# Kernel optimization log

Hardware: AMD Instinct MI355X
Metric: run time of the kernel (lower is better)

## Reference

```python
import jax, jax.numpy as jnp
import numpy as np

N = 512            # n_inputs (even)
L = N              # n_layers = n_inputs
PE = N // 2        # couplers per even column
PO = N // 2 - 1    # couplers per odd column
TWO_PI = 6.283185307179586


def _ste_clamp(theta):
    # clamp_ste: clamp value to [0, 2*pi], straight-through gradient
    c = jnp.clip(theta, 0.0, TWO_PI)
    return theta + jax.lax.stop_gradient(c - theta)


def _phase(theta):
    return jax.lax.complex(jnp.cos(theta), jnp.sin(theta))


def _pc_even(M, theta):
    # phase shifter on upper arm of each even pair: rows 0,2,4,...
    return M.at[0::2].multiply(_phase(theta)[:, None])


def _pc_odd(M, theta):
    # phase shifter on upper arm of each odd pair: rows 1,3,...,N-3
    return M.at[1:N - 1:2].multiply(_phase(theta)[:, None])


def _mmi_coeffs(loss, imb):
    # lossy, imbalanced 2x2 MMI: a*[[t, i r],[i r, t]]
    a = jnp.sqrt(1.0 - loss)
    t = a * jnp.sqrt(0.5 + imb)
    r = a * jnp.sqrt(0.5 - imb)
    ir = jax.lax.complex(jnp.zeros_like(r), r)
    return t, ir


def _mmi_even(M, loss, imb):
    t, ir = _mmi_coeffs(loss, imb)
    Mp = M.reshape(PE, 2, N)                       # pairs (0,1),(2,3),...
    top, bot = Mp[:, 0], Mp[:, 1]
    nt = t[:, None] * top + ir[:, None] * bot
    nb = ir[:, None] * top + t[:, None] * bot
    return jnp.stack([nt, nb], axis=1).reshape(N, N)


def _mmi_odd(M, loss, imb):
    t, ir = _mmi_coeffs(loss, imb)
    Mi = M[1:N - 1].reshape(PO, 2, N)              # pairs (1,2),(3,4),...
    top, bot = Mi[:, 0], Mi[:, 1]
    nt = t[:, None] * top + ir[:, None] * bot
    nb = ir[:, None] * top + t[:, None] * bot
    mid = jnp.stack([nt, nb], axis=1).reshape(N - 2, N)
    return jnp.concatenate([M[:1], mid, M[N - 1:]], axis=0)


def _forward(pc_even_phases, pc_odd_phases, pc_out_phases,
             mmi_loss_even, mmi_imb_even, mmi_loss_odd, mmi_imb_odd):
    pe = _ste_clamp(pc_even_phases).reshape(L // 2, 2, PE)
    po = _ste_clamp(pc_odd_phases).reshape(L // 2, 2, PO)
    le = mmi_loss_even.reshape(L // 2, 2, PE)
    ie = mmi_imb_even.reshape(L // 2, 2, PE)
    lo = mmi_loss_odd.reshape(L // 2, 2, PO)
    io = mmi_imb_odd.reshape(L // 2, 2, PO)

    def step(M, p):
        pe_, le_, ie_, po_, lo_, io_ = p
        for j in range(2):  # two even PC+MMI columns
            M = _pc_even(M, pe_[j])
            M = _mmi_even(M, le_[j], ie_[j])
        for j in range(2):  # two odd PC+MMI columns
            M = _pc_odd(M, po_[j])
            M = _mmi_odd(M, lo_[j], io_[j])
        return M, None

    M0 = jnp.eye(N, dtype=jnp.complex64)
    M, _ = jax.lax.scan(jax.checkpoint(step), M0, (pe, le, ie, po, lo, io))
    # output phase column on every wire
    return M * _phase(_ste_clamp(pc_out_phases))[:, None]


def setup_inputs() -> dict:
    key = jax.random.key(0)
    ks = jax.random.split(key, 7)
    return {
        "pc_even_phases": jax.random.uniform(ks[0], (L, PE), jnp.float32, 0.0, TWO_PI),
        "pc_odd_phases": jax.random.uniform(ks[1], (L, PO), jnp.float32, 0.0, TWO_PI),
        "pc_out_phases": jax.random.uniform(ks[2], (N,), jnp.float32, 0.0, TWO_PI),
        "mmi_loss_even": jax.random.uniform(ks[3], (L, PE), jnp.float32, 0.0, 0.05),
        "mmi_imb_even": jax.random.uniform(ks[4], (L, PE), jnp.float32, -0.05, 0.05),
        "mmi_loss_odd": jax.random.uniform(ks[5], (L, PO), jnp.float32, 0.0, 0.05),
        "mmi_imb_odd": jax.random.uniform(ks[6], (L, PO), jnp.float32, -0.05, 0.05),
    }


def reference(pc_even_phases, pc_odd_phases, pc_out_phases,
              mmi_loss_even, mmi_imb_even, mmi_loss_odd, mmi_imb_odd):
    return _forward(pc_even_phases, pc_odd_phases, pc_out_phases,
                    mmi_loss_even, mmi_imb_even, mmi_loss_odd, mmi_imb_odd)
```

## Files before the change

kernel.cpp:

```cpp
#include <hip/hip_runtime.h>
#include <hip/hip_fp16.h>

#define TWO_PI_F 6.283185307179586f

__device__ __forceinline__ float clamp02pi(float x) {
    return fminf(fmaxf(x, 0.0f), TWO_PI_F);
}

__device__ __forceinline__ float2 cmul(const float2 a, const float2 b) {
    return make_float2(a.x * b.x - a.y * b.y, a.x * b.y + a.y * b.x);
}
__device__ __forceinline__ float2 cadd(const float2 a, const float2 b) {
    return make_float2(a.x + b.x, a.y + b.y);
}
__device__ __forceinline__ float2 cscale(const float s, const float2 a) {
    return make_float2(s * a.x, s * a.y);
}
__device__ __forceinline__ float2 imul(const float r, const float2 e) {
    return make_float2(-r * e.y, r * e.x);
}
__device__ __forceinline__ float2 cfma(const float2 acc, const float2 a, const float2 b) {
    return make_float2(acc.x + a.x * b.x - a.y * b.y,
                       acc.y + a.x * b.y + a.y * b.x);
}

__device__ __forceinline__ float2 h2f(const unsigned u) {
    return __half22float2(__builtin_bit_cast(__half2, u));
}
__device__ __forceinline__ unsigned f2h(const float2 f) {
    return __builtin_bit_cast(unsigned, __float22half2_rn(f));
}

__device__ __forceinline__ void compose_row_w(
    const float4 (*sE)[72], const float4 (*sO)[72], const int r, const int P0,
    float4& h0, float4& h1)
{
    float2 f0, f1, f2, f3;
    if (r == 0) {
        const float4 q1 = sE[1][0], q0 = sE[0][0];
        const float2 e1 = make_float2(q1.x, q1.y);
        const float2 e0 = make_float2(q0.x, q0.y);
        const float2 v2 = cscale(q1.z, e1);
        const float2 v3 = make_float2(0.0f, q1.w);
        f2 = cadd(cmul(v2, cscale(q0.z, e0)), cmul(v3, imul(q0.w, e0)));
        f3 = cadd(cmul(v2, make_float2(0.0f, q0.w)), cscale(q0.z, v3));
        f0 = make_float2(0.0f, 0.0f);
        f1 = make_float2(0.0f, 0.0f);
    } else {
        const int pidx = ((r - 1) >> 1) - P0;
        const int qidx = min(((r - 1) >> 1) + 1, 255) - P0;
        const float4 qO1 = sO[1][pidx], qO0 = sO[0][pidx];
        const float2 eO1 = make_float2(qO1.x, qO1.y);
        const float2 eO0 = make_float2(qO0.x, qO0.y);
        float2 w1, w2;
        if (r & 1) { w1 = cscale(qO1.z, eO1); w2 = make_float2(0.0f, qO1.w); }
        else       { w1 = imul(qO1.w, eO1);   w2 = make_float2(qO1.z, 0.0f); }
        const float2 u1 = cadd(cmul(w1, cscale(qO0.z, eO0)),
                               cmul(w2, imul(qO0.w, eO0)));
        const float2 u2 = cadd(cmul(w1, make_float2(0.0f, qO0.w)),
                               cscale(qO0.z, w2));
        const float4 qE1p = sE[1][pidx], qE1q = sE[1][qidx];
        const float4 qE0p = sE[0][pidx], qE0q = sE[0][qidx];
        const float2 eE1p = make_float2(qE1p.x, qE1p.y);
        const float2 eE1q = make_float2(qE1q.x, qE1q.y);
        const float2 eE0p = make_float2(qE0p.x, qE0p.y);
        const float2 eE0q = make_float2(qE0q.x, qE0q.y);
        const float2 v0 = cmul(u1, imul(qE1p.w, eE1p));
        const float2 v1 = cscale(qE1p.z, u1);
        const float2 v2 = cmul(u2, cscale(qE1q.z, eE1q));
        const float2 v3 = cmul(u2, make_float2(0.0f, qE1q.w));
        f0 = cadd(cmul(v0, cscale(qE0p.z, eE0p)), cmul(v1, imul(qE0p.w, eE0p)));
        f1 = cadd(cmul(v0, make_float2(0.0f, qE0p.w)), cscale(qE0p.z, v1));
        f2 = cadd(cmul(v2, cscale(qE0q.z, eE0q)), cmul(v3, imul(qE0q.w, eE0q)));
        f3 = cadd(cmul(v2, make_float2(0.0f, qE0q.w)), cscale(qE0q.z, v3));
    }
    h0 = make_float4(f0.x, f0.y, f1.x, f1.y);
    h1 = make_float4(f2.x, f2.y, f3.x, f3.y);
}

__global__ __launch_bounds__(256) void compose8q_kernel(
    const float* __restrict__ pe, const float* __restrict__ po,
    const float* __restrict__ le, const float* __restrict__ ie,
    const float* __restrict__ lo, const float* __restrict__ io,
    uint4* __restrict__ Mch8)
{
    const int q = blockIdx.x;
    const int j = q >> 2;
    const int quarter = q & 3;
    const int R0 = 128 * quarter;
    const int P0 = (quarter == 0) ? 0 : ((R0 - 3) >> 1);
    const int t = threadIdx.x;

    __shared__ float4 sE[4][72];
    __shared__ float4 sO[4][72];
    __shared__ float4 B4[2][134][2];

    for (int it = t; it < 576; it += 256) {
        const int half = it / 288;
        const int rem  = it % 288;
        const int sub  = rem / 72;
        const int w    = rem % 72;
        const int p    = P0 + w;
        if (p > 255) continue;
        if (half == 0) {
            const int idx = (4 * j + sub) * 256 + p;
            float s, c;
            __sincosf(clamp02pi(pe[idx]), &s, &c);
            const float a = sqrtf(1.0f - le[idx]);
            sE[sub][w] = make_float4(c, s, a * sqrtf(0.5f + ie[idx]),
                                           a * sqrtf(0.5f - ie[idx]));
        } else {
            float4 qv = make_float4(1.0f, 0.0f, 1.0f, 0.0f);
            if (p < 255) {
                const int odx = (4 * j + sub) * 255 + p;
                float s, c;
                __sincosf(clamp02pi(po[odx]), &s, &c);
                const float a = sqrtf(1.0f - lo[odx]);
                qv = make_float4(c, s, a * sqrtf(0.5f + io[odx]),
                                       a * sqrtf(0.5f - io[odx]));
            }
            sO[sub][w] = qv;
        }
    }
    __syncthreads();

    for (int it = t; it < 268; it += 256) {
        const int s = it / 134, slot = it % 134;
        const int row = R0 - 2 + slot;
        if (row >= 0 && row <= 511) {
            float4 h0, h1;
            compose_row_w(&sE[2 * s], &sO[2 * s], row, P0, h0, h1);
            B4[s][slot][0] = h0;
            B4[s][slot][1] = h1;
        }
    }
    __syncthreads();

    if (t < 128) {
        const int r = R0 + t;
        const int base = (r & 1) ? (r - 1) : (r - 2);
        const int sr = t + 2;
        const float4 wv0 = B4[1][sr][0], wv1 = B4[1][sr][1];
        const float2 w0 = make_float2(wv0.x, wv0.y), w1 = make_float2(wv0.z, wv0.w);
        const float2 w2 = make_float2(wv1.x, wv1.y), w3 = make_float2(wv1.z, wv1.w);
        float2 p0 = make_float2(0.f,0.f), p1 = p0, p2 = p0, p3 = p0,
               p4 = p0, p5 = p0, p6 = p0, p7 = p0;
        {   const int k = min(max(base, 0), 511) - (R0 - 2);
            const float4 a = B4[0][k][0], b = B4[0][k][1];
            p0 = cfma(p0, w0, make_float2(a.x, a.y));
            p1 = cfma(p1, w0, make_float2(a.z, a.w));
            p2 = cfma(p2, w0, make_float2(b.x, b.y));
            p3 = cfma(p3, w0, make_float2(b.z, b.w)); }
        {   const int k = min(max(base + 1, 0), 511) - (R0 - 2);
            const float4 a = B4[0][k][0], b = B4[0][k][1];
            p2 = cfma(p2, w1, make_float2(a.x, a.y));
            p3 = cfma(p3, w1, make_float2(a.z, a.w));
            p4 = cfma(p4, w1, make_float2(b.x, b.y));
            p5 = cfma(p5, w1, make_float2(b.z, b.w)); }
        {   const int k = min(max(base + 2, 0), 511) - (R0 - 2);
            const float4 a = B4[0][k][0], b = B4[0][k][1];
            p2 = cfma(p2, w2, make_float2(a.x, a.y));
            p3 = cfma(p3, w2, make_float2(a.z, a.w));
            p4 = cfma(p4, w2, make_float2(b.x, b.y));
            p5 = cfma(p5, w2, make_float2(b.z, b.w)); }
        {   const int k = min(max(base + 3, 0), 511) - (R0 - 2);
            const float4 a = B4[0][k][0], b = B4[0][k][1];
            p4 = cfma(p4, w3, make_float2(a.x, a.y));
            p5 = cfma(p5, w3, make_float2(a.z, a.w));
            p6 = cfma(p6, w3, make_float2(b.x, b.y));
            p7 = cfma(p7, w3, make_float2(b.z, b.w)); }
        uint4* dst = Mch8 + (size_t)j * 1024 + (r & 1) * 512 + (r >> 1);
        dst[0]   = make_uint4(f2h(p0), f2h(p1), f2h(p2), f2h(p3));
        dst[256] = make_uint4(f2h(p4), f2h(p5), f2h(p6), f2h(p7));
    }
}

__device__ __forceinline__ float2 hrow4(const uint4 q, const float2 a,
                                        const float2 b, const float2 d,
                                        const float2 e, float2 acc)
{
    acc = cfma(acc, h2f(q.x), a);
    acc = cfma(acc, h2f(q.y), b);
    acc = cfma(acc, h2f(q.z), d);
    acc = cfma(acc, h2f(q.w), e);
    return acc;
}

__global__ __launch_bounds__(256) void mesh8h_kernel(
    const uint4* __restrict__ Mch,
    const float* __restrict__ pout,
    float* __restrict__ out, const int out_size)
{
    const int t   = threadIdx.x;
    const int col = blockIdx.x;

    __shared__ float4 S[2][260];

    float2 T = make_float2((2 * t     == col) ? 1.0f : 0.0f, 0.0f);
    float2 B = make_float2((2 * t + 1 == col) ? 1.0f : 0.0f, 0.0f);
    S[0][t + 2] = make_float4(T.x, T.y, B.x, B.y);
    if (t < 2) {
        const float4 z = make_float4(0.f, 0.f, 0.f, 0.f);
        S[0][t] = z; S[1][t] = z;
        S[0][258 + t] = z; S[1][258 + t] = z;
    }

    uint4 c0 = Mch[t],       c1 = Mch[256 + t],
          c2 = Mch[512 + t], c3 = Mch[768 + t];
    __syncthreads();

#pragma unroll 1
    for (int i = 0; i < 128; ++i) {
        const int nb = ((i + 1) & 127) * 1024 + t;
        const uint4 n0 = Mch[nb],       n1 = Mch[nb + 256],
                    n2 = Mch[nb + 512], n3 = Mch[nb + 768];

        const float4* SS = S[i & 1];
        const float4 s0 = SS[t], s1 = SS[t + 1], s3 = SS[t + 3], s4 = SS[t + 4];

        float2 YT = hrow4(c0, make_float2(s0.x, s0.y), make_float2(s0.z, s0.w),
                              make_float2(s1.x, s1.y), make_float2(s1.z, s1.w),
                          make_float2(0.f, 0.f));
        YT = hrow4(c1, T, B,
                       make_float2(s3.x, s3.y), make_float2(s3.z, s3.w), YT);
        float2 YB = hrow4(c2, make_float2(s1.x, s1.y), make_float2(s1.z, s1.w),
                              T, B, make_float2(0.f, 0.f));
        YB = hrow4(c3, make_float2(s3.x, s3.y), make_float2(s3.z, s3.w),
                       make_float2(s4.x, s4.y), make_float2(s4.z, s4.w), YB);
        T = YT; B = YB;
        S[(i + 1) & 1][t + 2] = make_float4(T.x, T.y, B.x, B.y);
        __syncthreads();

        c0 = n0; c1 = n1; c2 = n2; c3 = n3;
    }

    float s0p, c0p, s1p, c1p;
    __sincosf(clamp02pi(pout[2 * t]),     &s0p, &c0p);
    __sincosf(clamp02pi(pout[2 * t + 1]), &s1p, &c1p);
    const int i0 = (2 * t) * 512 + col;
    const int i1 = i0 + 512;
    if (i0 < out_size) out[i0] = c0p * T.x - s0p * T.y;
    if (i1 < out_size) out[i1] = c1p * B.x - s1p * B.y;
}

__global__ __launch_bounds__(256) void mesh_kernel(
    const float* __restrict__ pe, const float* __restrict__ po,
    const float* __restrict__ pout,
    const float* __restrict__ le, const float* __restrict__ ie,
    const float* __restrict__ lo, const float* __restrict__ io,
    float* __restrict__ out, const int out_size)
{
    const int p = threadIdx.x;
    const int b = blockIdx.x;

    __shared__ float4 P[2][256];

    P[0][p] = (p == b) ? make_float4(1.0f, 0.0f, 0.0f, 0.0f)
                       : make_float4(0.0f, 0.0f, 0.0f, 0.0f);
    P[1][p] = (p == b) ? make_float4(0.0f, 0.0f, 1.0f, 0.0f)
                       : make_float4(0.0f, 0.0f, 0.0f, 0.0f);

#pragma unroll 1
    for (int i = 0; i < 256; ++i) {
        const int e0 = (2 * i) * 256 + p, e1 = e0 + 256;
        const float pe0 = pe[e0], le0 = le[e0], ie0 = ie[e0];
        const float pe1 = pe[e1], le1 = le[e1], ie1 = ie[e1];
        float po0 = 0.0f, lo0 = 0.0f, io0 = 0.0f;
        float po1 = 0.0f, lo1 = 0.0f, io1 = 0.0f;
        if (p < 255) {
            const int o0 = (2 * i) * 255 + p, o1 = o0 + 255;
            po0 = po[o0]; lo0 = lo[o0]; io0 = io[o0];
            po1 = po[o1]; lo1 = lo[o1]; io1 = io[o1];
        }

        float4 v0 = P[0][p];
        float4 v1 = P[1][p];
#pragma unroll
        for (int j = 0; j < 2; ++j) {
            float s, c;
            __sincosf(clamp02pi(j ? pe1 : pe0), &s, &c);
            const float a  = sqrtf(1.0f - (j ? le1 : le0));
            const float tt = a * sqrtf(0.5f + (j ? ie1 : ie0));
            const float rr = a * sqrtf(0.5f - (j ? ie1 : ie0));
            {
                const float ptr_ = c * v0.x - s * v0.y;
                const float pti_ = c * v0.y + s * v0.x;
                v0 = make_float4(tt * ptr_ - rr * v0.w, tt * pti_ + rr * v0.z,
                                 tt * v0.z - rr * pti_, tt * v0.w + rr * ptr_);
            }
            {
                const float ptr_ = c * v1.x - s * v1.y;
                const float pti_ = c * v1.y + s * v1.x;
                v1 = make_float4(tt * ptr_ - rr * v1.w, tt * pti_ + rr * v1.z,
                                 tt * v1.z - rr * pti_, tt * v1.w + rr * ptr_);
            }
        }
        P[0][p] = v0;
        P[1][p] = v1;
        __syncthreads();

        if (p < 255) {
            float2 top0 = make_float2(P[0][p].z, P[0][p].w);
            float2 bot0 = make_float2(P[0][p + 1].x, P[0][p + 1].y);
            float2 top1 = make_float2(P[1][p].z, P[1][p].w);
            float2 bot1 = make_float2(P[1][p + 1].x, P[1][p + 1].y);
#pragma unroll
            for (int j = 0; j < 2; ++j) {
                float s, c;
                __sincosf(clamp02pi(j ? po1 : po0), &s, &c);
                const float a  = sqrtf(1.0f - (j ? lo1 : lo0));
                const float tt = a * sqrtf(0.5f + (j ? io1 : io0));
                const float rr = a * sqrtf(0.5f - (j ? io1 : io0));
                {
                    const float ptr_ = c * top0.x - s * top0.y;
                    const float pti_ = c * top0.y + s * top0.x;
                    const float nbx = tt * bot0.x - rr * pti_;
                    const float nby = tt * bot0.y + rr * ptr_;
                    top0 = make_float2(tt * ptr_ - rr * bot0.y, tt * pti_ + rr * bot0.x);
                    bot0 = make_float2(nbx, nby);
                }
                {
                    const float ptr_ = c * top1.x - s * top1.y;
                    const float pti_ = c * top1.y + s * top1.x;
                    const float nbx = tt * bot1.x - rr * pti_;
                    const float nby = tt * bot1.y + rr * ptr_;
                    top1 = make_float2(tt * ptr_ - rr * bot1.y, tt * pti_ + rr * bot1.x);
                    bot1 = make_float2(nbx, nby);
                }
            }
            P[0][p].z = top0.x; P[0][p].w = top0.y;
            P[0][p + 1].x = bot0.x; P[0][p + 1].y = bot0.y;
            P[1][p].z = top1.x; P[1][p].w = top1.y;
            P[1][p + 1].x = bot1.x; P[1][p + 1].y = bot1.y;
        }
        __syncthreads();
    }

    const float4 v0 = P[0][p];
    const float4 v1 = P[1][p];
    float s0, c0, s1, c1;
    __sincosf(clamp02pi(pout[2 * p]),     &s0, &c0);
    __sincosf(clamp02pi(pout[2 * p + 1]), &s1, &c1);

    float4 w0, w1;
    w0.x = c0 * v0.x - s0 * v0.y;  w0.y = c0 * v0.y + s0 * v0.x;
    w0.z = c0 * v1.x - s0 * v1.y;  w0.w = c0 * v1.y + s0 * v1.x;
    w1.x = c1 * v0.z - s1 * v0.w;  w1.y = c1 * v0.w + s1 * v0.z;
    w1.z = c1 * v1.z - s1 * v1.w;  w1.w = c1 * v1.w + s1 * v1.z;

    const int i0 = (2 * p) * 512 + 2 * b;
    const int i1 = (2 * p + 1) * 512 + 2 * b;
    if (i0 + 1 < out_size) *(float2*)(out + i0) = make_float2(w0.x, w0.z);
    if (i1 + 1 < out_size) *(float2*)(out + i1) = make_float2(w1.x, w1.z);
}

extern "C" void kernel_launch(void* const* d_in, const int* in_sizes, int n_in,
                              void* d_out, int out_size, void* d_ws, size_t ws_size,
                              hipStream_t stream)
{
    const float* pe   = (const float*)d_in[0];
    const float* po   = (const float*)d_in[1];
    const float* pout = (const float*)d_in[2];
    const float* le   = (const float*)d_in[3];
    const float* ie   = (const float*)d_in[4];
    const float* lo   = (const float*)d_in[5];
    const float* io   = (const float*)d_in[6];

    const size_t need = (size_t)128 * 1024 * sizeof(uint4);
    if (ws_size >= need) {
        uint4* Mch8 = (uint4*)d_ws;
        compose8q_kernel<<<512, 256, 0, stream>>>(pe, po, le, ie, lo, io, Mch8);
        mesh8h_kernel<<<512, 256, 0, stream>>>(Mch8, pout, (float*)d_out, out_size);
    } else {
        mesh_kernel<<<256, 256, 0, stream>>>(pe, po, pout, le, ie, lo, io,
                                             (float*)d_out, out_size);
    }
}
```

Baseline: 144.6 us.

## Assign one mesh row per thread with 512-thread blocks

The mesh application kernel now uses 512 threads per block, with each thread computing a single output row instead of a pair of rows. The compose kernel's output layout changes so each thread reads its two 8-coefficient half-precision chunks contiguously. The aim is twice the parallelism and fewer registers and loads per thread in the serial 128-step loop. In exchange, the per-step barrier now spans 512 threads and there are more shared-memory reads per output element.

```diff
diff --git a/kernel.cpp b/kernel.cpp
--- a/kernel.cpp
+++ b/kernel.cpp
@@ -169,9 +169,9 @@
             p5 = cfma(p5, w3, make_float2(a.z, a.w));
             p6 = cfma(p6, w3, make_float2(b.x, b.y));
             p7 = cfma(p7, w3, make_float2(b.z, b.w)); }
-        uint4* dst = Mch8 + (size_t)j * 1024 + (r & 1) * 512 + (r >> 1);
+        uint4* dst = Mch8 + (size_t)j * 1024 + r;
         dst[0]   = make_uint4(f2h(p0), f2h(p1), f2h(p2), f2h(p3));
-        dst[256] = make_uint4(f2h(p4), f2h(p5), f2h(p6), f2h(p7));
+        dst[512] = make_uint4(f2h(p4), f2h(p5), f2h(p6), f2h(p7));
     }
 }
 
@@ -186,61 +186,55 @@
     return acc;
 }
 
-__global__ __launch_bounds__(256) void mesh8h_kernel(
+__global__ __launch_bounds__(512) void mesh8r_kernel(
     const uint4* __restrict__ Mch,
     const float* __restrict__ pout,
     float* __restrict__ out, const int out_size)
 {
-    const int t   = threadIdx.x;
+    const int r   = threadIdx.x;
     const int col = blockIdx.x;
-
-    __shared__ float4 S[2][260];
-
-    float2 T = make_float2((2 * t     == col) ? 1.0f : 0.0f, 0.0f);
-    float2 B = make_float2((2 * t + 1 == col) ? 1.0f : 0.0f, 0.0f);
-    S[0][t + 2] = make_float4(T.x, T.y, B.x, B.y);
-    if (t < 2) {
+    const int t   = r >> 1;
+    const int odd = r & 1;
+
+    __shared__ float4 S[2][264];
+
+    float2 Y = make_float2((r == col) ? 1.0f : 0.0f, 0.0f);
+    ((float2*)&S[0][t + 2])[odd] = Y;
+    if (r < 2) {
         const float4 z = make_float4(0.f, 0.f, 0.f, 0.f);
-        S[0][t] = z; S[1][t] = z;
-        S[0][258 + t] = z; S[1][258 + t] = z;
-    }
-
-    uint4 c0 = Mch[t],       c1 = Mch[256 + t],
-          c2 = Mch[512 + t], c3 = Mch[768 + t];
+        S[0][r] = z; S[1][r] = z;
+        S[0][258 + r] = z; S[1][258 + r] = z;
+    }
+
+    uint4 c0 = Mch[r], c1 = Mch[512 + r];
     __syncthreads();
 
 #pragma unroll 1
     for (int i = 0; i < 128; ++i) {
-        const int nb = ((i + 1) & 127) * 1024 + t;
-        const uint4 n0 = Mch[nb],       n1 = Mch[nb + 256],
-                    n2 = Mch[nb + 512], n3 = Mch[nb + 768];
+        const int nb = ((i + 1) & 127) * 1024 + r;
+        const uint4 n0 = Mch[nb], n1 = Mch[nb + 512];
 
         const float4* SS = S[i & 1];
-        const float4 s0 = SS[t], s1 = SS[t + 1], s3 = SS[t + 3], s4 = SS[t + 4];
-
-        float2 YT = hrow4(c0, make_float2(s0.x, s0.y), make_float2(s0.z, s0.w),
-                              make_float2(s1.x, s1.y), make_float2(s1.z, s1.w),
-                          make_float2(0.f, 0.f));
-        YT = hrow4(c1, T, B,
-                       make_float2(s3.x, s3.y), make_float2(s3.z, s3.w), YT);
-        float2 YB = hrow4(c2, make_float2(s1.x, s1.y), make_float2(s1.z, s1.w),
-                              T, B, make_float2(0.f, 0.f));
-        YB = hrow4(c3, make_float2(s3.x, s3.y), make_float2(s3.z, s3.w),
-                       make_float2(s4.x, s4.y), make_float2(s4.z, s4.w), YB);
-        T = YT; B = YB;
-        S[(i + 1) & 1][t + 2] = make_float4(T.x, T.y, B.x, B.y);
+        const int b0 = t + odd;
+        const float4 q0 = SS[b0],     q1 = SS[b0 + 1],
+                     q2 = SS[b0 + 2], q3 = SS[b0 + 3];
+
+        Y = hrow4(c0, make_float2(q0.x, q0.y), make_float2(q0.z, q0.w),
+                      make_float2(q1.x, q1.y), make_float2(q1.z, q1.w),
+                  make_float2(0.f, 0.f));
+        Y = hrow4(c1, make_float2(q2.x, q2.y), make_float2(q2.z, q2.w),
+                      make_float2(q3.x, q3.y), make_float2(q3.z, q3.w), Y);
+
+        ((float2*)&S[(i + 1) & 1][t + 2])[odd] = Y;
         __syncthreads();
 
-        c0 = n0; c1 = n1; c2 = n2; c3 = n3;
-    }
-
-    float s0p, c0p, s1p, c1p;
-    __sincosf(clamp02pi(pout[2 * t]),     &s0p, &c0p);
-    __sincosf(clamp02pi(pout[2 * t + 1]), &s1p, &c1p);
-    const int i0 = (2 * t) * 512 + col;
-    const int i1 = i0 + 512;
-    if (i0 < out_size) out[i0] = c0p * T.x - s0p * T.y;
-    if (i1 < out_size) out[i1] = c1p * B.x - s1p * B.y;
+        c0 = n0; c1 = n1;
+    }
+
+    float s, c;
+    __sincosf(clamp02pi(pout[r]), &s, &c);
+    const int o = r * 512 + col;
+    if (o < out_size) out[o] = c * Y.x - s * Y.y;
 }
 
 __global__ __launch_bounds__(256) void mesh_kernel(
@@ -370,7 +364,7 @@
     if (ws_size >= need) {
         uint4* Mch8 = (uint4*)d_ws;
         compose8q_kernel<<<512, 256, 0, stream>>>(pe, po, le, ie, lo, io, Mch8);
-        mesh8h_kernel<<<512, 256, 0, stream>>>(Mch8, pout, (float*)d_out, out_size);
+        mesh8r_kernel<<<512, 512, 0, stream>>>(Mch8, pout, (float*)d_out, out_size);
     } else {
         mesh_kernel<<<256, 256, 0, stream>>>(pe, po, pout, le, ie, lo, io,
                                              (float*)d_out, out_size);
```

New measurement: 140.9 us. -2.6%, faster.
